# Optimization experiments

Measured on AMD Instinct MI355X. Metric: run time of the kernel, lower is better.

The kernel has to match this reference:

```python
import jax, jax.numpy as jnp
import numpy as np

B, S, H, E, T, V = 64, 80, 512, 512, 30, 32000


def setup_inputs() -> dict:
    key = jax.random.key(0)
    ks = jax.random.split(key, 16)
    sc = 0.02
    inp = {
        'encoder_output': jax.random.normal(ks[0], (B, S, H), jnp.float32),
        'targets': jax.random.randint(ks[1], (B, T), 0, V),
        'embedding': jax.random.normal(ks[2], (V, E), jnp.float32) * sc,
        # Attention MLP (note: no nonlinearities between W1/W2/W3 in the original)
        'W1': jax.random.normal(ks[3], (H, 2 * H), jnp.float32) * sc,
        'b1': jnp.zeros((H,), jnp.float32),
        'W2': jax.random.normal(ks[4], (H, H), jnp.float32) * sc,
        'b2': jnp.zeros((H,), jnp.float32),
        'W3': jax.random.normal(ks[5], (H, H), jnp.float32) * sc,
        'b3': jnp.zeros((H,), jnp.float32),
        'v_att': jax.random.normal(ks[6], (H,), jnp.float32) * sc,
        # GRU (torch gate order: r, z, n), input size H+E
        'W_ih': jax.random.normal(ks[7], (3 * H, H + E), jnp.float32) * sc,
        'b_ih': jnp.zeros((3 * H,), jnp.float32),
        'W_hh': jax.random.normal(ks[8], (3 * H, H), jnp.float32) * sc,
        'b_hh': jnp.zeros((3 * H,), jnp.float32),
        # Output projection to vocab
        'W_out': jax.random.normal(ks[9], (V, H), jnp.float32) * sc,
        'b_out': jnp.zeros((V,), jnp.float32),
    }
    return inp


def _decode(encoder_output, targets, embedding, W1, b1, W2, b2, W3, b3, v_att,
            W_ih, b_ih, W_hh, b_hh, W_out, b_out):
    h_dim = W_hh.shape[1]
    # Split W1 over the concat (encoder_outputs, hidden): same math as concat+linear
    W1_enc, W1_hid = W1[:, :h_dim], W1[:, h_dim:]
    enc_part = jnp.einsum('bsf,hf->bsh', encoder_output, W1_enc) + b1  # [B,S,H]

    tgt_emb = embedding[targets]                 # [B,T,E]
    xs = jnp.swapaxes(tgt_emb[:, :-1, :], 0, 1)  # [T-1,B,E], teacher forcing

    def step(h, emb_t):
        # Bahdanau-style attention (pure linear chain + softmax)
        x = enc_part + (h @ W1_hid.T)[:, None, :]          # [B,S,H]
        x = jnp.einsum('bsh,gh->bsg', x, W2) + b2
        x = jnp.einsum('bsh,gh->bsg', x, W3) + b3
        attn = jax.nn.softmax(jnp.einsum('bsh,h->bs', x, v_att), axis=1)
        context = jnp.einsum('bs,bsf->bf', attn, encoder_output)  # [B,H]
        # GRU cell, input = [embed, context]
        gx = jnp.concatenate([emb_t, context], axis=-1)
        gi = gx @ W_ih.T + b_ih
        gh = h @ W_hh.T + b_hh
        r = jax.nn.sigmoid(gi[:, :h_dim] + gh[:, :h_dim])
        z = jax.nn.sigmoid(gi[:, h_dim:2 * h_dim] + gh[:, h_dim:2 * h_dim])
        n = jnp.tanh(gi[:, 2 * h_dim:] + r * gh[:, 2 * h_dim:])
        h_new = (1.0 - z) * n + z * h
        logits = h_new @ W_out.T + b_out                   # [B,V]
        return h_new, logits

    h0 = jnp.zeros((encoder_output.shape[0], h_dim), encoder_output.dtype)
    _, logits = jax.lax.scan(step, h0, xs)                 # [T-1,B,V]
    return jnp.swapaxes(logits, 0, 1)                      # [B,T-1,V]


def reference(encoder_output, targets, embedding, W1, b1, W2, b2, W3, b3, v_att,
              W_ih, b_ih, W_hh, b_hh, W_out, b_out):
    seq_logProb = _decode(encoder_output, targets, embedding, W1, b1, W2, b2, W3,
                          b3, v_att, W_ih, b_ih, W_hh, b_hh, W_out, b_out)
    caption_preds = jnp.argmax(seq_logProb, axis=2)
    return seq_logProb, caption_preds
```

## Files before the change

### kernel.cpp

```cpp
#include <hip/hip_runtime.h>
#include <cstdint>
#include <cstddef>

#define B_  64
#define S_  80
#define H_  512
#define E_  512
#define T_  30
#define V_  32000
#define TD  (T_ - 1)
#define M_  (TD * B_)

typedef __attribute__((ext_vector_type(8))) short s16x8;
typedef __attribute__((ext_vector_type(4))) float f32x4;
typedef __attribute__((ext_vector_type(4))) unsigned short us16x4;

__device__ __forceinline__ unsigned short f2bf(float x) {
  unsigned u = __float_as_uint(x);
  return (unsigned short)((u + 0x7FFFu + ((u >> 16) & 1u)) >> 16);
}
__device__ __forceinline__ float bf2f(unsigned short h) {
  return __uint_as_float((unsigned)h << 16);
}

__device__ __forceinline__ void gld16(void* lds, const void* g) {
  __builtin_amdgcn_global_load_lds(
      (const __attribute__((address_space(1))) void*)g,
      (__attribute__((address_space(3))) void*)lds, 16, 0, 0);
}

__global__ __launch_bounds__(256) void k_split(
    const float* __restrict__ src, unsigned short* __restrict__ hi,
    unsigned short* __restrict__ lo, int n4) {
  int stride = gridDim.x * 256;
  for (int i = blockIdx.x * 256 + threadIdx.x; i < n4; i += stride) {
    float4 v = ((const float4*)src)[i];
    float x[4] = {v.x, v.y, v.z, v.w};
    us16x4 h, l;
#pragma unroll
    for (int q = 0; q < 4; ++q) {
      unsigned short hb = f2bf(x[q]);
      h[q] = hb;
      l[q] = f2bf(x[q] - bf2f(hb));
    }
    ((us16x4*)hi)[i] = h;
    ((us16x4*)lo)[i] = l;
  }
}

__global__ __launch_bounds__(512) void k_attn_vec(
    const float* __restrict__ W1, const float* __restrict__ W2,
    const float* __restrict__ W3, const float* __restrict__ v_att,
    float* __restrict__ wenc) {
  __shared__ float s_a[512];
  __shared__ float s_b[512];
  int t = threadIdx.x;
  s_a[t] = v_att[t];
  __syncthreads();
  float acc = 0.f;
  for (int g = 0; g < 512; ++g) acc += W3[g * 512 + t] * s_a[g];
  s_b[t] = acc;
  __syncthreads();
  acc = 0.f;
  for (int g = 0; g < 512; ++g) acc += W2[g * 512 + t] * s_b[g];
  s_a[t] = acc;
  __syncthreads();
  acc = 0.f;
  for (int h = 0; h < 512; ++h) acc += W1[h * 1024 + t] * s_a[h];
  wenc[t] = acc;
}

__global__ __launch_bounds__(512) void k_score_ctx(
    const float* __restrict__ enc, const float* __restrict__ wenc,
    float* __restrict__ context) {
  int b = blockIdx.x;
  int t = threadIdx.x;
  __shared__ float s_w[512];
  __shared__ float s_sc[80];
  __shared__ float s_at[80];
  __shared__ float s_mx, s_inv;
  s_w[t] = wenc[t];
  __syncthreads();
  int wave = t >> 6, lane = t & 63;
  for (int s = wave; s < S_; s += 8) {
    const float* row = enc + ((size_t)b * S_ + s) * 512;
    float acc = 0.f;
    for (int c = 0; c < 8; ++c) acc += row[lane + 64 * c] * s_w[lane + 64 * c];
    for (int off = 32; off; off >>= 1) acc += __shfl_down(acc, off);
    if (lane == 0) s_sc[s] = acc;
  }
  __syncthreads();
  if (t == 0) {
    float mx = -INFINITY;
    for (int s = 0; s < S_; ++s) mx = fmaxf(mx, s_sc[s]);
    s_mx = mx;
  }
  __syncthreads();
  if (t < S_) s_at[t] = expf(s_sc[t] - s_mx);
  __syncthreads();
  if (t == 0) {
    float sm = 0.f;
    for (int s = 0; s < S_; ++s) sm += s_at[s];
    s_inv = 1.f / sm;
  }
  __syncthreads();
  float inv = s_inv;
  float acc = 0.f;
  for (int s = 0; s < S_; ++s) acc += s_at[s] * enc[((size_t)b * S_ + s) * 512 + t];
  context[b * 512 + t] = acc * inv;
}

__global__ __launch_bounds__(256) void k_gctx(
    const float* __restrict__ context, const float* __restrict__ W_ih,
    const float* __restrict__ b_ih, float* __restrict__ gctx) {
  int b = blockIdx.x;
  int t = threadIdx.x;
  __shared__ float s_c[512];
  s_c[t] = context[b * 512 + t];
  s_c[t + 256] = context[b * 512 + 256 + t];
  __syncthreads();
  int wave = t >> 6, lane = t & 63;
  for (int i = 0; i < 16; ++i) {
    int j = blockIdx.y * 64 + wave * 16 + i;
    const float* row = W_ih + (size_t)j * 1024 + 512;
    float acc = 0.f;
    for (int c = 0; c < 8; ++c) acc += row[lane + 64 * c] * s_c[lane + 64 * c];
    for (int off = 32; off; off >>= 1) acc += __shfl_down(acc, off);
    if (lane == 0) gctx[b * 1536 + j] = acc + b_ih[j];
  }
}

__global__ __launch_bounds__(256) void k_giemb(
    const float* __restrict__ emb, const int* __restrict__ targets,
    const float* __restrict__ W_ih, const float* __restrict__ gctx,
    float* __restrict__ gic) {
  __shared__ float As[16][68];
  __shared__ float Bs[16][68];
  int m0 = blockIdx.x * 64;
  int j0 = blockIdx.y * 64;
  int t = threadIdx.x;
  int lr = t >> 2;
  int lk = (t & 3) * 4;
  int m = m0 + lr;
  int tt = m >> 6, bb = m & 63;
  const float* arow = emb + (size_t)targets[bb * T_ + tt] * 512;
  const float* brow = W_ih + (size_t)(j0 + lr) * 1024;
  int tx = t & 15, ty = t >> 4;
  float acc[4][4] = {};
  for (int k0 = 0; k0 < 512; k0 += 16) {
    float4 av = *(const float4*)(arow + k0 + lk);
    float4 bv = *(const float4*)(brow + k0 + lk);
    __syncthreads();
    As[lk + 0][lr] = av.x; As[lk + 1][lr] = av.y; As[lk + 2][lr] = av.z; As[lk + 3][lr] = av.w;
    Bs[lk + 0][lr] = bv.x; Bs[lk + 1][lr] = bv.y; Bs[lk + 2][lr] = bv.z; Bs[lk + 3][lr] = bv.w;
    __syncthreads();
    for (int kk = 0; kk < 16; ++kk) {
      float4 a4 = *(const float4*)&As[kk][ty * 4];
      float4 b4 = *(const float4*)&Bs[kk][tx * 4];
      float a[4] = {a4.x, a4.y, a4.z, a4.w};
      float bb4[4] = {b4.x, b4.y, b4.z, b4.w};
      for (int i = 0; i < 4; ++i)
        for (int j = 0; j < 4; ++j) acc[i][j] += a[i] * bb4[j];
    }
  }
  for (int i = 0; i < 4; ++i) {
    int mm = m0 + ty * 4 + i;
    int bb2 = mm & 63;
    float4 v;
    int jj = j0 + tx * 4;
    v.x = acc[i][0] + gctx[bb2 * 1536 + jj + 0];
    v.y = acc[i][1] + gctx[bb2 * 1536 + jj + 1];
    v.z = acc[i][2] + gctx[bb2 * 1536 + jj + 2];
    v.w = acc[i][3] + gctx[bb2 * 1536 + jj + 3];
    *(float4*)(gic + (size_t)mm * 1536 + jj) = v;
  }
}

__global__ __launch_bounds__(256) void k_step(
    const float* __restrict__ h_prev, const float* __restrict__ W_hh,
    const float* __restrict__ b_hh, const float* __restrict__ gic_t,
    float* __restrict__ h_out) {
  int b = blockIdx.x;
  int i0 = blockIdx.y * 64;
  int t = threadIdx.x;
  __shared__ float s_h[512];
  __shared__ float s_g[3][64];
  s_h[t] = h_prev[b * 512 + t];
  s_h[256 + t] = h_prev[b * 512 + 256 + t];
  __syncthreads();
  int wave = t >> 6, lane = t & 63;
  for (int d = wave; d < 192; d += 4) {
    int part = d >> 6;
    int ii = d & 63;
    int j = part * 512 + i0 + ii;
    const float* row = W_hh + (size_t)j * 512;
    float acc = 0.f;
    for (int c = 0; c < 8; ++c) acc += row[lane + 64 * c] * s_h[lane + 64 * c];
    for (int off = 32; off; off >>= 1) acc += __shfl_down(acc, off);
    if (lane == 0) s_g[part][ii] = acc + b_hh[j];
  }
  __syncthreads();
  if (t < 64) {
    int i = i0 + t;
    float gi_r = gic_t[b * 1536 + i];
    float gi_z = gic_t[b * 1536 + 512 + i];
    float gi_n = gic_t[b * 1536 + 1024 + i];
    float r = 1.f / (1.f + expf(-(gi_r + s_g[0][t])));
    float z = 1.f / (1.f + expf(-(gi_z + s_g[1][t])));
    float n = tanhf(gi_n + r * s_g[2][t]);
    h_out[b * 512 + i] = (1.f - z) * n + z * s_h[i];
  }
}

__global__ __launch_bounds__(256) void k_logits_mfma(
    const unsigned short* __restrict__ Ah, const unsigned short* __restrict__ Al,
    const unsigned short* __restrict__ Bh, const unsigned short* __restrict__ Bl,
    const float* __restrict__ b_out, float* __restrict__ out) {
  __shared__ unsigned short As_h[128 * 32], As_l[128 * 32];
  __shared__ unsigned short Bs_h[128 * 32], Bs_l[128 * 32];
  int t = threadIdx.x;
  int w = t >> 6, l = t & 63;
  int m0 = blockIdx.x * 128, n0 = blockIdx.y * 128;

  int c8 = (l & 3) * 8;
  int rr = (w << 4) + (l >> 2);
  int aoff[2], boff[2];
#pragma unroll
  for (int p = 0; p < 2; ++p) {
    int r = rr + (p << 6);
    int am = m0 + r; if (am >= M_) am = M_ - 1;
    aoff[p] = am * 512 + c8;
    boff[p] = (n0 + r) * 512 + c8;
  }

  int wr = (w >> 1) << 6;
  int wc = (w & 1) << 6;
  int lm = l & 15;
  int k8 = (l >> 4) << 3;
  f32x4 acc[4][4] = {};

  for (int k0 = 0; k0 < 512; k0 += 32) {
#pragma unroll
    for (int p = 0; p < 2; ++p) {
      int d = (p << 11) + (w << 9);
      gld16(&As_h[d], Ah + aoff[p] + k0);
      gld16(&As_l[d], Al + aoff[p] + k0);
      gld16(&Bs_h[d], Bh + boff[p] + k0);
      gld16(&Bs_l[d], Bl + boff[p] + k0);
    }
    __syncthreads();

    s16x8 ah[4], al[4], bh[4], bl[4];
#pragma unroll
    for (int i = 0; i < 4; ++i) {
      int ao = (wr + (i << 4) + lm) * 32 + k8;
      ah[i] = *(const s16x8*)&As_h[ao];
      al[i] = *(const s16x8*)&As_l[ao];
      int bo = (wc + (i << 4) + lm) * 32 + k8;
      bh[i] = *(const s16x8*)&Bs_h[bo];
      bl[i] = *(const s16x8*)&Bs_l[bo];
    }
#pragma unroll
    for (int i = 0; i < 4; ++i)
#pragma unroll
      for (int j = 0; j < 4; ++j) {
        acc[i][j] = __builtin_amdgcn_mfma_f32_16x16x32_bf16(ah[i], bh[j], acc[i][j], 0, 0, 0);
        acc[i][j] = __builtin_amdgcn_mfma_f32_16x16x32_bf16(ah[i], bl[j], acc[i][j], 0, 0, 0);
        acc[i][j] = __builtin_amdgcn_mfma_f32_16x16x32_bf16(al[i], bh[j], acc[i][j], 0, 0, 0);
      }
    __syncthreads();
  }

  float bo4[4];
#pragma unroll
  for (int j = 0; j < 4; ++j) bo4[j] = b_out[n0 + wc + (j << 4) + lm];
  int rq = (l >> 4) << 2;
#pragma unroll
  for (int i = 0; i < 4; ++i)
#pragma unroll
    for (int q = 0; q < 4; ++q) {
      int m = m0 + wr + (i << 4) + rq + q;
      if (m >= M_) continue;
      float* orow = out + ((size_t)(m & 63) * TD + (m >> 6)) * V_ + n0 + wc + lm;
#pragma unroll
      for (int j = 0; j < 4; ++j)
        orow[j << 4] = acc[i][j][q] + bo4[j];
    }
}

__global__ __launch_bounds__(256) void k_logits(
    const float* __restrict__ Hall, const float* __restrict__ W_out,
    const float* __restrict__ b_out, float* __restrict__ out) {
  __shared__ float As[8][132];
  __shared__ float Bs[8][132];
  int m0 = blockIdx.x * 128;
  int n0 = blockIdx.y * 128;
  int t = threadIdx.x;
  int lr = t >> 1;
  int lk = (t & 1) * 4;
  int am = m0 + lr;
  if (am >= M_) am = M_ - 1;
  const float* arow = Hall + (size_t)am * 512;
  const float* brow = W_out + (size_t)(n0 + lr) * 512;
  int tx = t & 15, ty = t >> 4;
  float acc[8][8] = {};
  for (int k0 = 0; k0 < 512; k0 += 8) {
    float4 av = *(const float4*)(arow + k0 + lk);
    float4 bv = *(const float4*)(brow + k0 + lk);
    __syncthreads();
    As[lk + 0][lr] = av.x; As[lk + 1][lr] = av.y; As[lk + 2][lr] = av.z; As[lk + 3][lr] = av.w;
    Bs[lk + 0][lr] = bv.x; Bs[lk + 1][lr] = bv.y; Bs[lk + 2][lr] = bv.z; Bs[lk + 3][lr] = bv.w;
    __syncthreads();
    for (int kk = 0; kk < 8; ++kk) {
      float4 a0 = *(const float4*)&As[kk][ty * 4];
      float4 a1 = *(const float4*)&As[kk][64 + ty * 4];
      float4 b0 = *(const float4*)&Bs[kk][tx * 4];
      float4 b1 = *(const float4*)&Bs[kk][64 + tx * 4];
      float a[8] = {a0.x, a0.y, a0.z, a0.w, a1.x, a1.y, a1.z, a1.w};
      float bb[8] = {b0.x, b0.y, b0.z, b0.w, b1.x, b1.y, b1.z, b1.w};
      for (int i = 0; i < 8; ++i)
        for (int j = 0; j < 8; ++j) acc[i][j] += a[i] * bb[j];
    }
  }
  for (int i = 0; i < 8; ++i) {
    int mm = m0 + ((i < 4) ? (ty * 4 + i) : (64 + ty * 4 + i - 4));
    if (mm >= M_) continue;
    size_t base = ((size_t)(mm & 63) * TD + (mm >> 6)) * V_;
    for (int half = 0; half < 2; ++half) {
      int nn = n0 + half * 64 + tx * 4;
      int jb = half * 4;
      float4 v;
      v.x = acc[i][jb + 0] + b_out[nn + 0];
      v.y = acc[i][jb + 1] + b_out[nn + 1];
      v.z = acc[i][jb + 2] + b_out[nn + 2];
      v.w = acc[i][jb + 3] + b_out[nn + 3];
      *(float4*)(out + base + nn) = v;
    }
  }
}

__global__ __launch_bounds__(256) void k_argmax(
    const float* __restrict__ out, float* __restrict__ preds) {
  const float* row = out + ((size_t)blockIdx.x * TD + blockIdx.y) * V_;
  int t = threadIdx.x;
  float best = -INFINITY;
  int bidx = 0x7fffffff;
  for (int v = t; v < V_; v += 256) {
    float x = row[v];
    if (x > best) { best = x; bidx = v; }
  }
  __shared__ float s_v[256];
  __shared__ int s_i[256];
  s_v[t] = best; s_i[t] = bidx;
  __syncthreads();
  for (int off = 128; off; off >>= 1) {
    if (t < off) {
      float v2 = s_v[t + off]; int i2 = s_i[t + off];
      if (v2 > s_v[t] || (v2 == s_v[t] && i2 < s_i[t])) { s_v[t] = v2; s_i[t] = i2; }
    }
    __syncthreads();
  }
  if (t == 0) preds[(size_t)blockIdx.x * TD + blockIdx.y] = (float)s_i[0];
}

extern "C" void kernel_launch(void* const* d_in, const int* in_sizes, int n_in,
                              void* d_out, int out_size, void* d_ws, size_t ws_size,
                              hipStream_t stream) {
  const float* enc   = (const float*)d_in[0];
  const int*   tgt   = (const int*)d_in[1];
  const float* emb   = (const float*)d_in[2];
  const float* W1    = (const float*)d_in[3];
  const float* W2    = (const float*)d_in[5];
  const float* W3    = (const float*)d_in[7];
  const float* v_att = (const float*)d_in[9];
  const float* W_ih  = (const float*)d_in[10];
  const float* b_ih  = (const float*)d_in[11];
  const float* W_hh  = (const float*)d_in[12];
  const float* b_hh  = (const float*)d_in[13];
  const float* W_out = (const float*)d_in[14];
  const float* b_out = (const float*)d_in[15];
  float* out = (float*)d_out;

  float* ws      = (float*)d_ws;
  float* wenc    = ws;
  float* context = wenc + 512;
  float* gctx    = context + 64 * 512;
  float* gic     = gctx + 64 * 1536;
  float* h0      = gic + (size_t)M_ * 1536;
  float* Hall    = h0 + 64 * 512;
  unsigned short* W_hi = (unsigned short*)(Hall + (size_t)M_ * 512);
  unsigned short* W_lo = W_hi + (size_t)V_ * 512;
  unsigned short* H_hi = W_lo + (size_t)V_ * 512;
  unsigned short* H_lo = H_hi + (size_t)M_ * 512;
  size_t need = (size_t)((char*)(H_lo + (size_t)M_ * 512) - (char*)d_ws);
  bool use_mfma = (ws_size >= need);

  if (use_mfma) {
    k_split<<<1024, 256, 0, stream>>>(W_out, W_hi, W_lo, V_ * 512 / 4);
  }

  hipMemsetAsync(h0, 0, 64 * 512 * sizeof(float), stream);
  k_attn_vec<<<1, 512, 0, stream>>>(W1, W2, W3, v_att, wenc);
  k_score_ctx<<<64, 512, 0, stream>>>(enc, wenc, context);
  k_gctx<<<dim3(64, 24), 256, 0, stream>>>(context, W_ih, b_ih, gctx);
  k_giemb<<<dim3(29, 24), 256, 0, stream>>>(emb, tgt, W_ih, gctx, gic);
  for (int t = 0; t < TD; ++t) {
    const float* hp = (t == 0) ? h0 : (Hall + (size_t)(t - 1) * 64 * 512);
    k_step<<<dim3(64, 8), 256, 0, stream>>>(hp, W_hh, b_hh,
                                            gic + (size_t)t * 64 * 1536,
                                            Hall + (size_t)t * 64 * 512);
  }
  if (use_mfma) {
    k_split<<<512, 256, 0, stream>>>(Hall, H_hi, H_lo, M_ * 512 / 4);
    k_logits_mfma<<<dim3(15, 250), 256, 0, stream>>>(H_hi, H_lo, W_hi, W_lo, b_out, out);
  } else {
    k_logits<<<dim3(15, 250), 256, 0, stream>>>(Hall, W_out, b_out, out);
  }
  k_argmax<<<dim3(64, TD), 256, 0, stream>>>(out, out + (size_t)M_ * V_);
}
```

Measured before the change: 1.445 ms.

## Fuse GRU recurrence into persistent cooperative kernel and swizzle logits tile order

Replaces 29 per-step GRU launches with one cooperative kernel of 64 blocks. Each block keeps its W_hh slice in shared memory as a bf16 hi/lo split and uses MFMA for the recurrent matmul, with a grid sync between timesteps. The kernel also writes the bf16 hi/lo hidden states directly, so the separate split pass is no longer needed. The logits GEMM grid is remapped to a grouped tile order for better L2 reuse of W_out. This removes launch overhead and repeated W_hh reads, but it depends on cooperative launch support and grid-sync cost, and uses 3-pass bf16 emulation for the recurrent matmul.

```diff
diff --git a/kernel.cpp b/kernel.cpp
--- a/kernel.cpp
+++ b/kernel.cpp
@@ -1,6 +1,9 @@
 #include <hip/hip_runtime.h>
+#include <hip/hip_cooperative_groups.h>
 #include <cstdint>
 #include <cstddef>
+
+namespace cg = cooperative_groups;
 
 #define B_  64
 #define S_  80
@@ -212,6 +215,107 @@
   }
 }
 
+__global__ __launch_bounds__(256) void k_gru_fused(
+    const float* __restrict__ W_hh, const float* __restrict__ b_hh,
+    const float* __restrict__ gic, float* __restrict__ Hall,
+    unsigned short* __restrict__ Hh, unsigned short* __restrict__ Hl) {
+  cg::grid_group grid = cg::this_grid();
+  __shared__ unsigned short sW[2][32][512];
+  int blk = blockIdx.x;
+  int i0 = blk * 8;
+  int t = threadIdx.x;
+  int l = t & 63;
+  int lm = l & 15;
+  int k8 = (l >> 4) << 3;
+
+  for (int idx = t; idx < 32 * 512; idx += 256) {
+    int row = idx >> 9, k = idx & 511;
+    float w = 0.f;
+    if (row < 8)       w = W_hh[(size_t)(i0 + row) * 512 + k];
+    else if (row < 16) w = W_hh[(size_t)(512 + i0 + row - 8) * 512 + k];
+    else if (row < 24) w = W_hh[(size_t)(1024 + i0 + row - 16) * 512 + k];
+    unsigned short hi = f2bf(w);
+    unsigned short lo = f2bf(w - bf2f(hi));
+    int byte = (k * 2) ^ ((row & 7) << 4);
+    *(unsigned short*)((char*)&sW[0][row][0] + byte) = hi;
+    *(unsigned short*)((char*)&sW[1][row][0] + byte) = lo;
+  }
+  float bhr = 0.f, bhz = 0.f, bhn = 0.f;
+  if (lm < 8) {
+    int i = i0 + lm;
+    bhr = b_hh[i]; bhz = b_hh[512 + i]; bhn = b_hh[1024 + i];
+  }
+  __syncthreads();
+
+  int arow[4];
+#pragma unroll
+  for (int mi = 0; mi < 4; ++mi) arow[mi] = (mi * 16 + lm) * 512 + k8;
+
+  for (int tt = 0; tt < TD; ++tt) {
+    f32x4 acc[4][2] = {};
+    if (tt > 0) {
+      const unsigned short* ah = Hh + (size_t)(tt - 1) * 64 * 512;
+      const unsigned short* al = Hl + (size_t)(tt - 1) * 64 * 512;
+      for (int k0 = 0; k0 < 512; k0 += 32) {
+        s16x8 a_h[4], a_l[4], b_h[2], b_l[2];
+#pragma unroll
+        for (int mi = 0; mi < 4; ++mi) {
+          a_h[mi] = *(const s16x8*)(ah + arow[mi] + k0);
+          a_l[mi] = *(const s16x8*)(al + arow[mi] + k0);
+        }
+        int byte = ((k0 + k8) * 2) ^ ((lm & 7) << 4);
+#pragma unroll
+        for (int g = 0; g < 2; ++g) {
+          b_h[g] = *(const s16x8*)((const char*)&sW[0][g * 16 + lm][0] + byte);
+          b_l[g] = *(const s16x8*)((const char*)&sW[1][g * 16 + lm][0] + byte);
+        }
+#pragma unroll
+        for (int mi = 0; mi < 4; ++mi)
+#pragma unroll
+          for (int g = 0; g < 2; ++g) {
+            acc[mi][g] = __builtin_amdgcn_mfma_f32_16x16x32_bf16(a_h[mi], b_h[g], acc[mi][g], 0, 0, 0);
+            acc[mi][g] = __builtin_amdgcn_mfma_f32_16x16x32_bf16(a_h[mi], b_l[g], acc[mi][g], 0, 0, 0);
+            acc[mi][g] = __builtin_amdgcn_mfma_f32_16x16x32_bf16(a_l[mi], b_h[g], acc[mi][g], 0, 0, 0);
+          }
+      }
+    }
+    const float* gict = gic + (size_t)tt * 64 * 1536;
+    float* hall_t = Hall + (size_t)tt * 64 * 512;
+    const float* hall_p = Hall + (size_t)(tt - 1) * 64 * 512;
+    unsigned short* hh_t = Hh + (size_t)tt * 64 * 512;
+    unsigned short* hl_t = Hl + (size_t)tt * 64 * 512;
+#pragma unroll
+    for (int mi = 0; mi < 4; ++mi)
+#pragma unroll
+      for (int q = 0; q < 4; ++q) {
+        float zraw = __shfl(acc[mi][0][q], l + 8);
+        if (lm < 8) {
+          int b = mi * 16 + ((l >> 4) << 2) + q;
+          int i = i0 + lm;
+          float ghr = acc[mi][0][q] + bhr;
+          float ghz = zraw + bhz;
+          float ghn = acc[mi][1][q] + bhn;
+          float gir = gict[b * 1536 + i];
+          float giz = gict[b * 1536 + 512 + i];
+          float gin = gict[b * 1536 + 1024 + i];
+          float hp = (tt == 0) ? 0.f : hall_p[b * 512 + i];
+          float r = 1.f / (1.f + expf(-(gir + ghr)));
+          float z = 1.f / (1.f + expf(-(giz + ghz)));
+          float n = tanhf(gin + r * ghn);
+          float h = (1.f - z) * n + z * hp;
+          hall_t[b * 512 + i] = h;
+          unsigned short hhi = f2bf(h);
+          hh_t[b * 512 + i] = hhi;
+          hl_t[b * 512 + i] = f2bf(h - bf2f(hhi));
+        }
+      }
+    if (tt + 1 < TD) {
+      __threadfence();
+      grid.sync();
+    }
+  }
+}
+
 __global__ __launch_bounds__(256) void k_logits_mfma(
     const unsigned short* __restrict__ Ah, const unsigned short* __restrict__ Al,
     const unsigned short* __restrict__ Bh, const unsigned short* __restrict__ Bl,
@@ -220,7 +324,14 @@
   __shared__ unsigned short Bs_h[128 * 32], Bs_l[128 * 32];
   int t = threadIdx.x;
   int w = t >> 6, l = t & 63;
-  int m0 = blockIdx.x * 128, n0 = blockIdx.y * 128;
+
+  int D = blockIdx.x;
+  int g = D / 120;
+  int loc = D - g * 120;
+  int bx, by;
+  if (g < 31) { by = g * 8 + (loc & 7); bx = loc >> 3; }
+  else        { by = 248 + (loc & 1);   bx = loc >> 1; }
+  int m0 = bx * 128, n0 = by * 128;
 
   int c8 = (l & 3) * 8;
   int rr = (w << 4) + (l >> 2);
@@ -399,20 +510,32 @@
     k_split<<<1024, 256, 0, stream>>>(W_out, W_hi, W_lo, V_ * 512 / 4);
   }
 
-  hipMemsetAsync(h0, 0, 64 * 512 * sizeof(float), stream);
   k_attn_vec<<<1, 512, 0, stream>>>(W1, W2, W3, v_att, wenc);
   k_score_ctx<<<64, 512, 0, stream>>>(enc, wenc, context);
   k_gctx<<<dim3(64, 24), 256, 0, stream>>>(context, W_ih, b_ih, gctx);
   k_giemb<<<dim3(29, 24), 256, 0, stream>>>(emb, tgt, W_ih, gctx, gic);
-  for (int t = 0; t < TD; ++t) {
-    const float* hp = (t == 0) ? h0 : (Hall + (size_t)(t - 1) * 64 * 512);
-    k_step<<<dim3(64, 8), 256, 0, stream>>>(hp, W_hh, b_hh,
-                                            gic + (size_t)t * 64 * 1536,
-                                            Hall + (size_t)t * 64 * 512);
-  }
+
+  bool chain_done = false;
   if (use_mfma) {
-    k_split<<<512, 256, 0, stream>>>(Hall, H_hi, H_lo, M_ * 512 / 4);
-    k_logits_mfma<<<dim3(15, 250), 256, 0, stream>>>(H_hi, H_lo, W_hi, W_lo, b_out, out);
+    void* kargs[] = {(void*)&W_hh, (void*)&b_hh, (void*)&gic, (void*)&Hall,
+                     (void*)&H_hi, (void*)&H_lo};
+    hipError_t e = hipLaunchCooperativeKernel((const void*)k_gru_fused,
+                                              dim3(64), dim3(256), kargs, 0, stream);
+    chain_done = (e == hipSuccess);
+  }
+  if (!chain_done) {
+    hipMemsetAsync(h0, 0, 64 * 512 * sizeof(float), stream);
+    for (int t = 0; t < TD; ++t) {
+      const float* hp = (t == 0) ? h0 : (Hall + (size_t)(t - 1) * 64 * 512);
+      k_step<<<dim3(64, 8), 256, 0, stream>>>(hp, W_hh, b_hh,
+                                              gic + (size_t)t * 64 * 1536,
+                                              Hall + (size_t)t * 64 * 512);
+    }
+    if (use_mfma) k_split<<<512, 256, 0, stream>>>(Hall, H_hi, H_lo, M_ * 512 / 4);
+  }
+
+  if (use_mfma) {
+    k_logits_mfma<<<dim3(3750), 256, 0, stream>>>(H_hi, H_lo, W_hi, W_lo, b_out, out);
   } else {
     k_logits<<<dim3(15, 250), 256, 0, stream>>>(Hall, W_out, b_out, out);
   }
```

Measured after the change: 1.941 ms. +34.4%, slower.
